# Optimization experiments

Hardware: AMD Instinct MI355X
Metric: run time of the kernel (lower is better)

The kernel has to match this reference:

```python
import jax, jax.numpy as jnp
import numpy as np

N_POINTS = 4000000
RESOLUTION = 512
HASHMAP_SIZE = 1 << 19  # 2**log2_hashmap_size
N_FEATURES = 4
# Instant-NGP style spatial-hash primes
PRIME_X = np.uint32(1)
PRIME_Y = np.uint32(2654435761)
PRIME_Z = np.uint32(805459861)


def setup_inputs() -> dict:
    key = jax.random.key(0)
    k1, k2 = jax.random.split(key)
    inputs = jax.random.randint(k1, (N_POINTS, 3), 0, RESOLUTION, dtype=jnp.int32)
    embeddings = jax.random.normal(k2, (HASHMAP_SIZE, N_FEATURES), dtype=jnp.float32)
    return {"inputs": inputs, "embeddings": embeddings,
            "resolution": RESOLUTION, "hashmap_size": HASHMAP_SIZE}


def _hash_index(coords_u32, hashmap_size):
    # coords_u32: [N,3] uint32; XOR-of-products spatial hash, modulo table size
    h = (coords_u32[:, 0] * PRIME_X) ^ (coords_u32[:, 1] * PRIME_Y) ^ (coords_u32[:, 2] * PRIME_Z)
    return (h % np.uint32(hashmap_size)).astype(jnp.int32)


def reference(inputs, embeddings, resolution, hashmap_size):
    # cnt_np_embed forward (axis='xy'):
    #   gather binarized (STE sign) embeddings by spatial hash of 3D int coords,
    #   scatter-count +1/-1 occurrences into a [scale, scale, F, 2] plane grid,
    #   then normalize to per-cell fractions (Bernoulli probabilities).
    scale = resolution - 2
    idx = _hash_index(inputs.astype(jnp.uint32), hashmap_size)      # [N]
    emb = embeddings[idx]                                           # [N, F] irregular gather
    # STE_binary forward: clamp then sign -> {-1, +1}
    b = jnp.where(emb >= 0, 1.0, -1.0).astype(emb.dtype)            # [N, F]
    pos = (1.0 + b) * 0.5                                           # 1 where +1
    neg = (1.0 - b) * 0.5                                           # 1 where -1
    # project onto the xy plane; clip coords into the (resolution-2)^2 grid
    u = jnp.clip(inputs[:, 0], 0, scale - 1)
    v = jnp.clip(inputs[:, 1], 0, scale - 1)
    cell = (u * scale + v).astype(jnp.int32)                        # [N]
    num_cells = scale * scale
    pn_pos = jax.ops.segment_sum(pos, cell, num_segments=num_cells)  # [S*S, F]
    pn_neg = jax.ops.segment_sum(neg, cell, num_segments=num_cells)  # [S*S, F]
    pn = jnp.stack([pn_pos, pn_neg], axis=-1).reshape(scale, scale, -1, 2)
    pn_sum = jnp.sum(pn, axis=-1, keepdims=True) + 1e-6
    return pn / pn_sum
```

## Files before the change

kernel.cpp:

```cpp
#include <hip/hip_runtime.h>

#define SCALE   510
#define NCELLS  (SCALE * SCALE)
#define NF      4
#define PRIME_Y 2654435761u
#define PRIME_Z 805459861u

#define NBKT    256
#define NBLK1   512
#define CAP     64
#define P1T     1024
#define P2T     1024
#define LDSROW  258

__global__ void signtab_kernel(const float4* __restrict__ emb,
                               unsigned char* __restrict__ signtab,
                               unsigned int hsize) {
    unsigned int i = blockIdx.x * blockDim.x + threadIdx.x;
    if (i * 2 >= hsize) return;
    float4 e0 = emb[2 * i + 0];
    float4 e1 = emb[2 * i + 1];
    unsigned int b = 0;
    if (e0.x >= 0.0f) b |= 1u << 0;
    if (e0.y >= 0.0f) b |= 1u << 1;
    if (e0.z >= 0.0f) b |= 1u << 2;
    if (e0.w >= 0.0f) b |= 1u << 3;
    if (e1.x >= 0.0f) b |= 1u << 4;
    if (e1.y >= 0.0f) b |= 1u << 5;
    if (e1.z >= 0.0f) b |= 1u << 6;
    if (e1.w >= 0.0f) b |= 1u << 7;
    signtab[i] = (unsigned char)b;
}

__device__ __forceinline__ void bin_point(
        int x, int y, int z,
        const unsigned char* __restrict__ signtab,
        unsigned short* __restrict__ seg,
        unsigned int* rank, unsigned int hmask) {
    unsigned int bkt = ((unsigned int)x >> 1) & (NBKT - 1u);
    unsigned int h = (unsigned int)x
                   ^ ((unsigned int)y * PRIME_Y)
                   ^ ((unsigned int)z * PRIME_Z);
    unsigned int idx  = h & hmask;
    unsigned int byte = signtab[idx >> 1];
    unsigned int nib  = (byte >> ((idx & 1u) * 4u)) & 0xFu;
    int u = min(max(x, 0), SCALE - 1);
    int v = min(max(y, 0), SCALE - 1);
    unsigned int rec = ((unsigned int)(u & 1) << 13)
                     | ((unsigned int)v << 4) | nib;
    unsigned int r = atomicAdd(&rank[bkt], 1u);
    if (r < CAP)
        seg[r * LDSROW + bkt] = (unsigned short)rec;
}

__global__ __launch_bounds__(P1T)
void binscatter_kernel(const int* __restrict__ inputs,
                       const unsigned char* __restrict__ signtab,
                       unsigned short* __restrict__ recs,
                       unsigned short* __restrict__ cntg,
                       int n, unsigned int hmask) {
    __shared__ unsigned int   rank[NBKT];
    __shared__ unsigned short seg[CAP * LDSROW];
    const int t = threadIdx.x, b = blockIdx.x;
    if (t < NBKT) rank[t] = 0;
    __syncthreads();

    const int nquad = n >> 2;
    const int qpb = (nquad + NBLK1 - 1) / NBLK1;
    const int q0 = b * qpb;
    const int q1 = min(q0 + qpb, nquad);
    const int4* in4 = (const int4*)inputs;
    for (int q = q0 + t; q < q1; q += P1T) {
        int4 A = in4[3 * q + 0];
        int4 B = in4[3 * q + 1];
        int4 C = in4[3 * q + 2];
        bin_point(A.x, A.y, A.z, signtab, seg, rank, hmask);
        bin_point(A.w, B.x, B.y, signtab, seg, rank, hmask);
        bin_point(B.z, B.w, C.x, signtab, seg, rank, hmask);
        bin_point(C.y, C.z, C.w, signtab, seg, rank, hmask);
    }
    if (b == 0 && t == 0) {
        for (int p = nquad * 4; p < n; ++p)
            bin_point(inputs[3 * p], inputs[3 * p + 1], inputs[3 * p + 2],
                      signtab, seg, rank, hmask);
    }
    __syncthreads();

    unsigned int* gout = (unsigned int*)(recs + (size_t)b * NBKT * CAP);
    for (int g2 = t; g2 < NBKT * CAP / 2; g2 += P1T) {
        int g   = g2 * 2;
        int bkt = g >> 6;
        int r   = g & 63;
        unsigned int lo = seg[r * LDSROW + bkt];
        unsigned int hi = seg[(r + 1) * LDSROW + bkt];
        gout[g2] = lo | (hi << 16);
    }
    if (t < NBKT)
        cntg[t * NBLK1 + b] = (unsigned short)min(rank[t], (unsigned int)CAP);
}

__device__ __forceinline__ void hist_add(unsigned long long* hist,
                                         unsigned int rec) {
    unsigned int nib = rec & 0xFu;
    unsigned int v   = (rec >> 4) & 0x1FFu;
    unsigned int ul  = rec >> 13;
    unsigned long long add = 1ull
        | ((unsigned long long)(nib & 1u)        << 12)
        | ((unsigned long long)((nib >> 1) & 1u) << 24)
        | ((unsigned long long)((nib >> 2) & 1u) << 36)
        | ((unsigned long long)((nib >> 3) & 1u) << 48);
    atomicAdd(&hist[ul * SCALE + v], add);
}

__global__ __launch_bounds__(P2T)
void histnorm_kernel(const unsigned short* __restrict__ recs,
                     const unsigned short* __restrict__ cntg,
                     float* __restrict__ out) {
    __shared__ unsigned long long hist[2 * SCALE];
    __shared__ unsigned short cl[NBLK1];
    const int t = threadIdx.x, b = blockIdx.x;
    for (int i = t; i < 2 * SCALE; i += P2T) hist[i] = 0;

    const int nreg = (b == 254) ? 2 : 1;
    for (int reg = 0; reg < nreg; ++reg) {
        const int bkt = reg ? 255 : b;
        if (t < NBLK1) cl[t] = cntg[bkt * NBLK1 + t];
        __syncthreads();
        for (int j = t; j < NBLK1 * CAP / 2; j += P2T) {
            const int s  = j >> 5;
            const int r0 = (j & 31) * 2;
            const unsigned int* segp = (const unsigned int*)
                (recs + ((size_t)s * NBKT + bkt) * CAP);
            unsigned int w = segp[j & 31];
            const int c = cl[s];
            if (r0 < c)     hist_add(hist, w & 0xFFFFu);
            if (r0 + 1 < c) hist_add(hist, w >> 16);
        }
        __syncthreads();
    }

    const size_t outbase = (size_t)(2 * b) * SCALE * 8;
    for (int c = t; c < 2 * SCALE; c += P2T) {
        unsigned long long vv = hist[c];
        float cc = (float)(unsigned int)(vv & 0xFFFull);
        float p0 = (float)(unsigned int)((vv >> 12) & 0xFFFull);
        float p1 = (float)(unsigned int)((vv >> 24) & 0xFFFull);
        float p2 = (float)(unsigned int)((vv >> 36) & 0xFFFull);
        float p3 = (float)(unsigned int)((vv >> 48) & 0xFFFull);
        float inv = 1.0f / (cc + 1e-6f);
        float4 o0, o1;
        o0.x = p0 * inv; o0.y = (cc - p0) * inv;
        o0.z = p1 * inv; o0.w = (cc - p1) * inv;
        o1.x = p2 * inv; o1.y = (cc - p2) * inv;
        o1.z = p3 * inv; o1.w = (cc - p3) * inv;
        float4* op = (float4*)(out + outbase + (size_t)c * 8);
        op[0] = o0;
        op[1] = o1;
    }
}

__global__ void scatter_fb_kernel(const int* __restrict__ inputs,
                                  const float4* __restrict__ emb,
                                  unsigned long long* __restrict__ cnt,
                                  int n, unsigned int hmask) {
    int i = blockIdx.x * blockDim.x + threadIdx.x;
    if (i >= n) return;
    int x = inputs[3 * i], y = inputs[3 * i + 1], z = inputs[3 * i + 2];
    unsigned int h = (unsigned int)x ^ ((unsigned int)y * PRIME_Y)
                   ^ ((unsigned int)z * PRIME_Z);
    float4 e = emb[h & hmask];
    unsigned long long add = 1ull;
    if (e.x >= 0.0f) add |= 1ull << 12;
    if (e.y >= 0.0f) add |= 1ull << 24;
    if (e.z >= 0.0f) add |= 1ull << 36;
    if (e.w >= 0.0f) add |= 1ull << 48;
    int u = min(max(x, 0), SCALE - 1);
    int v = min(max(y, 0), SCALE - 1);
    atomicAdd(&cnt[u * SCALE + v], add);
}

__global__ void normalize_fb_kernel(const unsigned long long* __restrict__ cnt,
                                    float* __restrict__ out) {
    int i = blockIdx.x * blockDim.x + threadIdx.x;
    if (i >= NCELLS) return;
    unsigned long long v = cnt[i];
    float c  = (float)(unsigned int)(v & 0xFFFull);
    float p0 = (float)(unsigned int)((v >> 12) & 0xFFFull);
    float p1 = (float)(unsigned int)((v >> 24) & 0xFFFull);
    float p2 = (float)(unsigned int)((v >> 36) & 0xFFFull);
    float p3 = (float)(unsigned int)((v >> 48) & 0xFFFull);
    float inv = 1.0f / (c + 1e-6f);
    float4 o0, o1;
    o0.x = p0 * inv; o0.y = (c - p0) * inv;
    o0.z = p1 * inv; o0.w = (c - p1) * inv;
    o1.x = p2 * inv; o1.y = (c - p2) * inv;
    o1.z = p3 * inv; o1.w = (c - p3) * inv;
    float4* outv = (float4*)(out + (size_t)i * 8);
    outv[0] = o0; outv[1] = o1;
}

extern "C" void kernel_launch(void* const* d_in, const int* in_sizes, int n_in,
                              void* d_out, int out_size, void* d_ws, size_t ws_size,
                              hipStream_t stream) {
    const int*    inputs = (const int*)d_in[0];
    const float4* emb    = (const float4*)d_in[1];
    int n = in_sizes[0] / 3;
    unsigned int hsize = (unsigned int)(in_sizes[1] / NF);
    unsigned int hmask = hsize - 1;

    const size_t recs_bytes = (size_t)NBLK1 * NBKT * CAP * 2;
    const size_t cnt_bytes  = (size_t)NBKT * NBLK1 * 2;
    const size_t sign_bytes = (size_t)hsize / 2;
    const size_t need       = recs_bytes + cnt_bytes + sign_bytes;

    const int threads = 256;
    if (ws_size >= need) {
        unsigned short* recs    = (unsigned short*)d_ws;
        unsigned short* cntg    = (unsigned short*)((char*)d_ws + recs_bytes);
        unsigned char*  signtab = (unsigned char*)d_ws + recs_bytes + cnt_bytes;

        signtab_kernel<<<((int)(hsize / 2) + threads - 1) / threads, threads,
                         0, stream>>>(emb, signtab, hsize);
        binscatter_kernel<<<NBLK1, P1T, 0, stream>>>(
            inputs, signtab, recs, cntg, n, hmask);
        histnorm_kernel<<<255, P2T, 0, stream>>>(recs, cntg, (float*)d_out);
    } else {
        unsigned long long* cnt = (unsigned long long*)d_ws;
        hipMemsetAsync(cnt, 0, (size_t)NCELLS * 8, stream);
        scatter_fb_kernel<<<(n + threads - 1) / threads, threads, 0, stream>>>(
            inputs, emb, cnt, n, hmask);
        normalize_fb_kernel<<<(NCELLS + threads - 1) / threads, threads, 0, stream>>>(
            cnt, (float*)d_out);
    }
}
```

Measured before the change: 50.47 us.

## Stage sign table halves in LDS with two-pass binning and global spill overflow

The 256 KB packed sign table is split into two 128 KB halves, and each half is copied into dynamic LDS in turn. Every block therefore reads its input slice twice and, in each pass, bins only the points whose hash falls in the resident half, so the random sign lookups hit LDS instead of L2. Per-bucket capacity drops from 64 to 48 to fit the larger LDS budget, and overflowing records now go to a global spill list that the histogram kernel scans. This fixes the earlier silent drop of records past capacity, at the cost of doubled input reads, a scan of the spill list in every histogram block, and a requirement that the table has 2^19 entries.

After: 49.59 us. About the same (-1.8%).

```diff
diff --git a/kernel.cpp b/kernel.cpp
--- a/kernel.cpp
+++ b/kernel.cpp
@@ -8,15 +8,23 @@
 
 #define NBKT    256
 #define NBLK1   512
-#define CAP     64
+#define CAP     48
 #define P1T     1024
 #define P2T     1024
-#define LDSROW  258
+#define LDSROW2 264
+#define TBLW    32768
+#define SPILLCAP 65536
+
+#define SEG_OFF  131072
+#define RANK_OFF (SEG_OFF + CAP * LDSROW2 * 2)
+#define DYNLDS   (RANK_OFF + NBKT * 4)
 
 __global__ void signtab_kernel(const float4* __restrict__ emb,
                                unsigned char* __restrict__ signtab,
+                               unsigned int* __restrict__ spillcnt,
                                unsigned int hsize) {
     unsigned int i = blockIdx.x * blockDim.x + threadIdx.x;
+    if (i == 0) *spillcnt = 0;
     if (i * 2 >= hsize) return;
     float4 e0 = emb[2 * i + 0];
     float4 e1 = emb[2 * i + 1];
@@ -32,67 +40,87 @@
     signtab[i] = (unsigned char)b;
 }
 
-__device__ __forceinline__ void bin_point(
-        int x, int y, int z,
-        const unsigned char* __restrict__ signtab,
+__device__ __forceinline__ void bin_point_lds(
+        int x, int y, int z, unsigned int pass,
+        const unsigned int* __restrict__ tbl,
         unsigned short* __restrict__ seg,
-        unsigned int* rank, unsigned int hmask) {
-    unsigned int bkt = ((unsigned int)x >> 1) & (NBKT - 1u);
+        unsigned int* __restrict__ rank,
+        unsigned int* __restrict__ spillcnt,
+        unsigned int* __restrict__ spill,
+        unsigned int hmask) {
     unsigned int h = (unsigned int)x
                    ^ ((unsigned int)y * PRIME_Y)
                    ^ ((unsigned int)z * PRIME_Z);
-    unsigned int idx  = h & hmask;
-    unsigned int byte = signtab[idx >> 1];
-    unsigned int nib  = (byte >> ((idx & 1u) * 4u)) & 0xFu;
+    unsigned int idx = h & hmask;
+    if ((idx >> 18) != pass) return;
+    unsigned int loc = idx & 0x3FFFFu;
+    unsigned int nib = (tbl[loc >> 3] >> ((loc & 7u) * 4u)) & 0xFu;
     int u = min(max(x, 0), SCALE - 1);
     int v = min(max(y, 0), SCALE - 1);
+    unsigned int bkt = ((unsigned int)x >> 1) & (NBKT - 1u);
     unsigned int rec = ((unsigned int)(u & 1) << 13)
                      | ((unsigned int)v << 4) | nib;
     unsigned int r = atomicAdd(&rank[bkt], 1u);
-    if (r < CAP)
-        seg[r * LDSROW + bkt] = (unsigned short)rec;
+    if (r < CAP) {
+        seg[r * LDSROW2 + bkt] = (unsigned short)rec;
+    } else {
+        unsigned int rs = atomicAdd(spillcnt, 1u);
+        if (rs < SPILLCAP) spill[rs] = (bkt << 16) | rec;
+    }
 }
 
 __global__ __launch_bounds__(P1T)
 void binscatter_kernel(const int* __restrict__ inputs,
-                       const unsigned char* __restrict__ signtab,
+                       const unsigned int* __restrict__ sig32,
                        unsigned short* __restrict__ recs,
                        unsigned short* __restrict__ cntg,
+                       unsigned int* __restrict__ spillcnt,
+                       unsigned int* __restrict__ spill,
                        int n, unsigned int hmask) {
-    __shared__ unsigned int   rank[NBKT];
-    __shared__ unsigned short seg[CAP * LDSROW];
+    extern __shared__ char smem[];
+    unsigned int*   tbl  = (unsigned int*)smem;
+    unsigned short* seg  = (unsigned short*)(smem + SEG_OFF);
+    unsigned int*   rank = (unsigned int*)(smem + RANK_OFF);
     const int t = threadIdx.x, b = blockIdx.x;
+
     if (t < NBKT) rank[t] = 0;
-    __syncthreads();
 
     const int nquad = n >> 2;
     const int qpb = (nquad + NBLK1 - 1) / NBLK1;
     const int q0 = b * qpb;
     const int q1 = min(q0 + qpb, nquad);
     const int4* in4 = (const int4*)inputs;
-    for (int q = q0 + t; q < q1; q += P1T) {
-        int4 A = in4[3 * q + 0];
-        int4 B = in4[3 * q + 1];
-        int4 C = in4[3 * q + 2];
-        bin_point(A.x, A.y, A.z, signtab, seg, rank, hmask);
-        bin_point(A.w, B.x, B.y, signtab, seg, rank, hmask);
-        bin_point(B.z, B.w, C.x, signtab, seg, rank, hmask);
-        bin_point(C.y, C.z, C.w, signtab, seg, rank, hmask);
-    }
-    if (b == 0 && t == 0) {
-        for (int p = nquad * 4; p < n; ++p)
-            bin_point(inputs[3 * p], inputs[3 * p + 1], inputs[3 * p + 2],
-                      signtab, seg, rank, hmask);
+
+    for (unsigned int pass = 0; pass < 2; ++pass) {
+        __syncthreads();
+        const uint4* src = (const uint4*)(sig32 + pass * TBLW);
+        uint4* dst = (uint4*)tbl;
+        for (int i = t; i < TBLW / 4; i += P1T) dst[i] = src[i];
+        __syncthreads();
+
+        for (int q = q0 + t; q < q1; q += P1T) {
+            int4 A = in4[3 * q + 0];
+            int4 B = in4[3 * q + 1];
+            int4 C = in4[3 * q + 2];
+            bin_point_lds(A.x, A.y, A.z, pass, tbl, seg, rank, spillcnt, spill, hmask);
+            bin_point_lds(A.w, B.x, B.y, pass, tbl, seg, rank, spillcnt, spill, hmask);
+            bin_point_lds(B.z, B.w, C.x, pass, tbl, seg, rank, spillcnt, spill, hmask);
+            bin_point_lds(C.y, C.z, C.w, pass, tbl, seg, rank, spillcnt, spill, hmask);
+        }
+        if (b == 0 && t == 0) {
+            for (int p = nquad * 4; p < n; ++p)
+                bin_point_lds(inputs[3 * p], inputs[3 * p + 1], inputs[3 * p + 2],
+                              pass, tbl, seg, rank, spillcnt, spill, hmask);
+        }
     }
     __syncthreads();
 
     unsigned int* gout = (unsigned int*)(recs + (size_t)b * NBKT * CAP);
     for (int g2 = t; g2 < NBKT * CAP / 2; g2 += P1T) {
-        int g   = g2 * 2;
-        int bkt = g >> 6;
-        int r   = g & 63;
-        unsigned int lo = seg[r * LDSROW + bkt];
-        unsigned int hi = seg[(r + 1) * LDSROW + bkt];
+        int bkt = g2 / (CAP / 2);
+        int r   = (g2 % (CAP / 2)) * 2;
+        unsigned int lo = seg[r * LDSROW2 + bkt];
+        unsigned int hi = seg[(r + 1) * LDSROW2 + bkt];
         gout[g2] = lo | (hi << 16);
     }
     if (t < NBKT)
@@ -115,26 +143,34 @@
 __global__ __launch_bounds__(P2T)
 void histnorm_kernel(const unsigned short* __restrict__ recs,
                      const unsigned short* __restrict__ cntg,
+                     const unsigned int* __restrict__ spillcnt,
+                     const unsigned int* __restrict__ spill,
                      float* __restrict__ out) {
     __shared__ unsigned long long hist[2 * SCALE];
     __shared__ unsigned short cl[NBLK1];
     const int t = threadIdx.x, b = blockIdx.x;
     for (int i = t; i < 2 * SCALE; i += P2T) hist[i] = 0;
+    const unsigned int nspill = min(*spillcnt, (unsigned int)SPILLCAP);
 
     const int nreg = (b == 254) ? 2 : 1;
     for (int reg = 0; reg < nreg; ++reg) {
-        const int bkt = reg ? 255 : b;
+        const unsigned int bkt = reg ? 255u : (unsigned int)b;
         if (t < NBLK1) cl[t] = cntg[bkt * NBLK1 + t];
         __syncthreads();
         for (int j = t; j < NBLK1 * CAP / 2; j += P2T) {
-            const int s  = j >> 5;
-            const int r0 = (j & 31) * 2;
+            const int s    = j / (CAP / 2);
+            const int widx = j % (CAP / 2);
+            const int r0   = widx * 2;
             const unsigned int* segp = (const unsigned int*)
                 (recs + ((size_t)s * NBKT + bkt) * CAP);
-            unsigned int w = segp[j & 31];
+            unsigned int w = segp[widx];
             const int c = cl[s];
             if (r0 < c)     hist_add(hist, w & 0xFFFFu);
             if (r0 + 1 < c) hist_add(hist, w >> 16);
+        }
+        for (unsigned int k = t; k < nspill; k += P2T) {
+            unsigned int w = spill[k];
+            if ((w >> 16) == bkt) hist_add(hist, w & 0xFFFFu);
         }
         __syncthreads();
     }
@@ -208,22 +244,31 @@
     unsigned int hsize = (unsigned int)(in_sizes[1] / NF);
     unsigned int hmask = hsize - 1;
 
-    const size_t recs_bytes = (size_t)NBLK1 * NBKT * CAP * 2;
-    const size_t cnt_bytes  = (size_t)NBKT * NBLK1 * 2;
-    const size_t sign_bytes = (size_t)hsize / 2;
-    const size_t need       = recs_bytes + cnt_bytes + sign_bytes;
+    const size_t recs_bytes  = (size_t)NBLK1 * NBKT * CAP * 2;
+    const size_t cntg_bytes  = (size_t)NBKT * NBLK1 * 2;
+    const size_t sign_bytes  = (size_t)hsize / 2;
+    const size_t spill_bytes = 64 + (size_t)SPILLCAP * 4;
+    const size_t need = recs_bytes + cntg_bytes + sign_bytes + spill_bytes;
 
     const int threads = 256;
-    if (ws_size >= need) {
-        unsigned short* recs    = (unsigned short*)d_ws;
-        unsigned short* cntg    = (unsigned short*)((char*)d_ws + recs_bytes);
-        unsigned char*  signtab = (unsigned char*)d_ws + recs_bytes + cnt_bytes;
+    if (ws_size >= need && hsize == (1u << 19)) {
+        char* w = (char*)d_ws;
+        unsigned short* recs    = (unsigned short*)w;
+        unsigned short* cntg    = (unsigned short*)(w + recs_bytes);
+        unsigned char*  signtab = (unsigned char*)(w + recs_bytes + cntg_bytes);
+        unsigned int*   spillc  = (unsigned int*)(w + recs_bytes + cntg_bytes + sign_bytes);
+        unsigned int*   spill   = spillc + 16;
+
+        hipFuncSetAttribute((const void*)binscatter_kernel,
+                            hipFuncAttributeMaxDynamicSharedMemorySize, DYNLDS);
 
         signtab_kernel<<<((int)(hsize / 2) + threads - 1) / threads, threads,
-                         0, stream>>>(emb, signtab, hsize);
-        binscatter_kernel<<<NBLK1, P1T, 0, stream>>>(
-            inputs, signtab, recs, cntg, n, hmask);
-        histnorm_kernel<<<255, P2T, 0, stream>>>(recs, cntg, (float*)d_out);
+                         0, stream>>>(emb, signtab, spillc, hsize);
+        binscatter_kernel<<<NBLK1, P1T, DYNLDS, stream>>>(
+            inputs, (const unsigned int*)signtab, recs, cntg, spillc, spill,
+            n, hmask);
+        histnorm_kernel<<<255, P2T, 0, stream>>>(recs, cntg, spillc, spill,
+                                                 (float*)d_out);
     } else {
         unsigned long long* cnt = (unsigned long long*)d_ws;
         hipMemsetAsync(cnt, 0, (size_t)NCELLS * 8, stream);
```
